# Kernel tuning notes

Hardware: AMD Instinct MI355X
Metric: run time of the kernel (lower is better)

## Reference

```python
import jax, jax.numpy as jnp
import numpy as np

B, NC, D, H, W = 2, 5, 96, 160, 160


def setup_inputs() -> dict:
    key = jax.random.key(0)
    k1, k2, k3 = jax.random.split(key, 3)
    source_logits = jax.random.normal(k1, (B, NC, D, H, W), dtype=jnp.float32)
    target_logits = jax.random.normal(k2, (B, NC, D, H, W), dtype=jnp.float32)
    gt = jax.random.randint(k3, (B, 1, D, H, W), 0, NC, dtype=jnp.int64)
    return {"source_logits": source_logits, "target_logits": target_logits, "gt": gt}


def reference(source_logits, target_logits, gt):
    temperature = 2.0
    eps = 1e-6
    n_class = source_logits.shape[1]
    batch = source_logits.shape[0]

    g = gt[:, 0]  # [B, D, H, W]
    # one-hot over classes: [K, B, D, H, W] (K = n_class segment ids)
    onehot = (g[None] == jnp.arange(n_class)[:, None, None, None, None]).astype(source_logits.dtype)
    # total voxel count per class over the whole batch (matches torch.sum(gt == i))
    nvox = jnp.sum(onehot, axis=(1, 2, 3, 4))  # [K]

    # per-class, per-batch, per-channel masked sums: single pass instead of n_class passes
    s_sum = jnp.einsum('kbdhw,bcdhw->kbc', onehot, source_logits)  # [K, B, C]
    t_sum = jnp.einsum('kbdhw,bcdhw->kbc', onehot, target_logits)

    denom = (nvox + eps)[:, None, None]
    s_avg = s_sum[:, :, 1:] / denom  # [K, B, C-1] (channel 0 dropped as in original)
    t_avg = t_sum[:, :, 1:] / denom

    s_lp = jax.nn.log_softmax(s_avg / temperature, axis=-1)
    t_lp = jax.nn.log_softmax(t_avg / temperature, axis=-1)

    # KLDivLoss(reduction='batchmean', log_target=True): sum(exp(t)*(t-s)) / batch
    kl_st = jnp.sum(jnp.exp(t_lp) * (t_lp - s_lp), axis=(1, 2)) / batch  # per class
    kl_ts = jnp.sum(jnp.exp(s_lp) * (s_lp - t_lp), axis=(1, 2)) / batch

    return jnp.mean((kl_st + kl_ts) / 2.0)
```

## Files before the change

kernel.cpp:

```cpp
#include <hip/hip_runtime.h>

#define NCLASS 5
#define NB 2
#define VOX (96*160*160)
#define V4  (VOX/4)
#define SLOTS 64
#define VALS  110
#define STAGP 1271


__global__ __launch_bounds__(256)
void kd_partial(const float* __restrict__ src, const float* __restrict__ tgt,
                const int* __restrict__ gt, float* __restrict__ ws)
{
    const int nbPerB = gridDim.x >> 1;
    const int b      = blockIdx.x / nbPerB;
    const int blk    = blockIdx.x - b * nbPerB;

    const float* sb = src + (size_t)b * NCLASS * VOX;
    const float* tb = tgt + (size_t)b * NCLASS * VOX;
    const int*   gb = gt  + (size_t)b * VOX;

    float accS[NCLASS][NCLASS];
    float accT[NCLASS][NCLASS];
    float cnt[NCLASS];
    #pragma unroll
    for (int k = 0; k < NCLASS; ++k) {
        cnt[k] = 0.f;
        #pragma unroll
        for (int c = 0; c < NCLASS; ++c) { accS[k][c] = 0.f; accT[k][c] = 0.f; }
    }

    const int tid    = blk * 256 + threadIdx.x;
    const int stride = nbPerB * 256;

    for (int i = tid; i < V4; i += stride) {
        #pragma unroll
        for (int c = 0; c < NCLASS; ++c) {
            int ic = i + c * STAGP;
            if (ic >= V4) ic -= V4;
            const int4   g4 = ((const int4*)gb)[ic];
            const float4 s4 = ((const float4*)(sb + (size_t)c * VOX))[ic];
            const float4 t4 = ((const float4*)(tb + (size_t)c * VOX))[ic];

            #define ACC_COMP(GX, SX, TX)                                     \
                { _Pragma("unroll")                                          \
                  for (int kk = 0; kk < NCLASS; ++kk) {                      \
                      const float m = ((GX) == kk) ? 1.0f : 0.0f;            \
                      accS[kk][c] = fmaf(m, (SX), accS[kk][c]);              \
                      accT[kk][c] = fmaf(m, (TX), accT[kk][c]);              \
                  } }
            ACC_COMP(g4.x, s4.x, t4.x)
            ACC_COMP(g4.y, s4.y, t4.y)
            ACC_COMP(g4.z, s4.z, t4.z)
            ACC_COMP(g4.w, s4.w, t4.w)
            #undef ACC_COMP

            if (c == 0) {
                #pragma unroll
                for (int kk = 0; kk < NCLASS; ++kk) {
                    cnt[kk] += ((g4.x == kk) ? 1.f : 0.f) + ((g4.y == kk) ? 1.f : 0.f)
                             + ((g4.z == kk) ? 1.f : 0.f) + ((g4.w == kk) ? 1.f : 0.f);
                }
            }
        }
    }

    __shared__ float lacc[55];
    const int lane = threadIdx.x & 63;
    if (threadIdx.x < 55) lacc[threadIdx.x] = 0.f;
    __syncthreads();

    #define WAVE_RED(VAL, IDX) {                                             \
        float v_ = (VAL);                                                    \
        _Pragma("unroll")                                                    \
        for (int off_ = 32; off_; off_ >>= 1) v_ += __shfl_xor(v_, off_);    \
        if (lane == 0) atomicAdd(&lacc[(IDX)], v_);                          \
    }
    #pragma unroll
    for (int k = 0; k < NCLASS; ++k) {
        #pragma unroll
        for (int c = 0; c < NCLASS; ++c) {
            WAVE_RED(accS[k][c], k * 5 + c);
            WAVE_RED(accT[k][c], 25 + k * 5 + c);
        }
        WAVE_RED(cnt[k], 50 + k);
    }
    #undef WAVE_RED
    __syncthreads();

    if (threadIdx.x < 55) {
        const int i = threadIdx.x;
        int gidx;
        if (i < 25)       gidx = b * 25 + i;
        else if (i < 50)  gidx = 50 + b * 25 + (i - 25);
        else              gidx = 100 + b * 5 + (i - 50);
        atomicAdd(&ws[(blockIdx.x & (SLOTS - 1)) * VALS + gidx], lacc[i]);
    }
}

__global__ void kd_final(const float* __restrict__ ws, float* __restrict__ out)
{
    const int tid = threadIdx.x;
    __shared__ float tot[VALS];

    for (int v = tid; v < VALS; v += 64) {
        float s = 0.f;
        #pragma unroll 8
        for (int slot = 0; slot < SLOTS; ++slot) s += ws[slot * VALS + v];
        tot[v] = s;
    }
    __syncthreads();

    const int l = (tid < 40) ? tid : 0;
    const int g = l >> 2;
    const int k = g >> 1;
    const int b = g & 1;
    const int c = l & 3;

    const double denom = (double)tot[100 + 0 * 5 + k]
                       + (double)tot[100 + 1 * 5 + k] + 1e-6;
    double sa = ((double)tot[(b * 5 + k) * 5 + (c + 1)] / denom) * 0.5;
    double ta = ((double)tot[50 + (b * 5 + k) * 5 + (c + 1)] / denom) * 0.5;

    double ms = sa, mt = ta;
    ms = fmax(ms, __shfl_xor(ms, 1)); ms = fmax(ms, __shfl_xor(ms, 2));
    mt = fmax(mt, __shfl_xor(mt, 1)); mt = fmax(mt, __shfl_xor(mt, 2));
    double es = exp(sa - ms), et = exp(ta - mt);
    es += __shfl_xor(es, 1); es += __shfl_xor(es, 2);
    et += __shfl_xor(et, 1); et += __shfl_xor(et, 2);
    const double slp = sa - (ms + log(es));
    const double tlp = ta - (mt + log(et));

    double term = exp(tlp) * (tlp - slp) + exp(slp) * (slp - tlp);
    if (tid >= 40) term = 0.0;

    #pragma unroll
    for (int off = 32; off; off >>= 1) term += __shfl_xor(term, off);
    if (tid == 0) out[0] = (float)(term / 20.0);
}

extern "C" void kernel_launch(void* const* d_in, const int* in_sizes, int n_in,
                              void* d_out, int out_size, void* d_ws, size_t ws_size,
                              hipStream_t stream)
{
    const float* src = (const float*)d_in[0];
    const float* tgt = (const float*)d_in[1];
    const int*   gt  = (const int*)d_in[2];
    float* out = (float*)d_out;
    float* ws  = (float*)d_ws;

    hipMemsetAsync(ws, 0, SLOTS * VALS * sizeof(float), stream);
    kd_partial<<<dim3(2048), dim3(256), 0, stream>>>(src, tgt, gt, ws);
    kd_final<<<dim3(1), dim3(64), 0, stream>>>(ws, out);
}
```

Baseline: 280.1 us.

## Split work per (batch, channel) slab to cut per-thread accumulators

```diff
diff --git a/kernel.cpp b/kernel.cpp
--- a/kernel.cpp
+++ b/kernel.cpp
@@ -6,96 +6,84 @@
 #define V4  (VOX/4)
 #define SLOTS 64
 #define VALS  110
-#define STAGP 1271
+#define BLKS_PER_SLAB 256
 
 
 __global__ __launch_bounds__(256)
 void kd_partial(const float* __restrict__ src, const float* __restrict__ tgt,
                 const int* __restrict__ gt, float* __restrict__ ws)
 {
-    const int nbPerB = gridDim.x >> 1;
-    const int b      = blockIdx.x / nbPerB;
-    const int blk    = blockIdx.x - b * nbPerB;
+    const int b = blockIdx.y / NCLASS;
+    const int c = blockIdx.y % NCLASS;
 
-    const float* sb = src + (size_t)b * NCLASS * VOX;
-    const float* tb = tgt + (size_t)b * NCLASS * VOX;
+    const float* sb = src + ((size_t)b * NCLASS + c) * VOX;
+    const float* tb = tgt + ((size_t)b * NCLASS + c) * VOX;
     const int*   gb = gt  + (size_t)b * VOX;
 
-    float accS[NCLASS][NCLASS];
-    float accT[NCLASS][NCLASS];
-    float cnt[NCLASS];
-    #pragma unroll
-    for (int k = 0; k < NCLASS; ++k) {
-        cnt[k] = 0.f;
-        #pragma unroll
-        for (int c = 0; c < NCLASS; ++c) { accS[k][c] = 0.f; accT[k][c] = 0.f; }
-    }
+    float accS[NCLASS] = {0.f, 0.f, 0.f, 0.f, 0.f};
+    float accT[NCLASS] = {0.f, 0.f, 0.f, 0.f, 0.f};
+    float cnt[NCLASS]  = {0.f, 0.f, 0.f, 0.f, 0.f};
 
-    const int tid    = blk * 256 + threadIdx.x;
-    const int stride = nbPerB * 256;
+    const int tid    = blockIdx.x * 256 + threadIdx.x;
+    const int stride = BLKS_PER_SLAB * 256;
 
-    for (int i = tid; i < V4; i += stride) {
-        #pragma unroll
-        for (int c = 0; c < NCLASS; ++c) {
-            int ic = i + c * STAGP;
-            if (ic >= V4) ic -= V4;
-            const int4   g4 = ((const int4*)gb)[ic];
-            const float4 s4 = ((const float4*)(sb + (size_t)c * VOX))[ic];
-            const float4 t4 = ((const float4*)(tb + (size_t)c * VOX))[ic];
+    #define BODY(WITH_CNT)                                                    \
+        for (int i = tid; i < V4; i += stride) {                              \
+            const int4   g4 = ((const int4*)gb)[i];                           \
+            const float4 s4 = ((const float4*)sb)[i];                         \
+            const float4 t4 = ((const float4*)tb)[i];                         \
+            _Pragma("unroll")                                                 \
+            for (int kk = 0; kk < NCLASS; ++kk) {                             \
+                const float mx = (g4.x == kk) ? 1.f : 0.f;                    \
+                const float my = (g4.y == kk) ? 1.f : 0.f;                    \
+                const float mz = (g4.z == kk) ? 1.f : 0.f;                    \
+                const float mw = (g4.w == kk) ? 1.f : 0.f;                    \
+                accS[kk] = fmaf(mx, s4.x, accS[kk]);                          \
+                accS[kk] = fmaf(my, s4.y, accS[kk]);                          \
+                accS[kk] = fmaf(mz, s4.z, accS[kk]);                          \
+                accS[kk] = fmaf(mw, s4.w, accS[kk]);                          \
+                accT[kk] = fmaf(mx, t4.x, accT[kk]);                          \
+                accT[kk] = fmaf(my, t4.y, accT[kk]);                          \
+                accT[kk] = fmaf(mz, t4.z, accT[kk]);                          \
+                accT[kk] = fmaf(mw, t4.w, accT[kk]);                          \
+                if (WITH_CNT) cnt[kk] += mx + my + mz + mw;                   \
+            }                                                                 \
+        }
+    if (c == 0) { BODY(1) } else { BODY(0) }
+    #undef BODY
 
-            #define ACC_COMP(GX, SX, TX)                                     \
-                { _Pragma("unroll")                                          \
-                  for (int kk = 0; kk < NCLASS; ++kk) {                      \
-                      const float m = ((GX) == kk) ? 1.0f : 0.0f;            \
-                      accS[kk][c] = fmaf(m, (SX), accS[kk][c]);              \
-                      accT[kk][c] = fmaf(m, (TX), accT[kk][c]);              \
-                  } }
-            ACC_COMP(g4.x, s4.x, t4.x)
-            ACC_COMP(g4.y, s4.y, t4.y)
-            ACC_COMP(g4.z, s4.z, t4.z)
-            ACC_COMP(g4.w, s4.w, t4.w)
-            #undef ACC_COMP
-
-            if (c == 0) {
-                #pragma unroll
-                for (int kk = 0; kk < NCLASS; ++kk) {
-                    cnt[kk] += ((g4.x == kk) ? 1.f : 0.f) + ((g4.y == kk) ? 1.f : 0.f)
-                             + ((g4.z == kk) ? 1.f : 0.f) + ((g4.w == kk) ? 1.f : 0.f);
-                }
-            }
-        }
-    }
-
-    __shared__ float lacc[55];
+    __shared__ float lacc[15];
     const int lane = threadIdx.x & 63;
-    if (threadIdx.x < 55) lacc[threadIdx.x] = 0.f;
+    if (threadIdx.x < 15) lacc[threadIdx.x] = 0.f;
     __syncthreads();
 
-    #define WAVE_RED(VAL, IDX) {                                             \
-        float v_ = (VAL);                                                    \
-        _Pragma("unroll")                                                    \
-        for (int off_ = 32; off_; off_ >>= 1) v_ += __shfl_xor(v_, off_);    \
-        if (lane == 0) atomicAdd(&lacc[(IDX)], v_);                          \
+    #define WAVE_RED(VAL, IDX) {                                              \
+        float v_ = (VAL);                                                     \
+        _Pragma("unroll")                                                     \
+        for (int off_ = 32; off_; off_ >>= 1) v_ += __shfl_xor(v_, off_);     \
+        if (lane == 0) atomicAdd(&lacc[(IDX)], v_);                           \
     }
     #pragma unroll
-    for (int k = 0; k < NCLASS; ++k) {
+    for (int kk = 0; kk < NCLASS; ++kk) {
+        WAVE_RED(accS[kk], kk);
+        WAVE_RED(accT[kk], 5 + kk);
+    }
+    if (c == 0) {
         #pragma unroll
-        for (int c = 0; c < NCLASS; ++c) {
-            WAVE_RED(accS[k][c], k * 5 + c);
-            WAVE_RED(accT[k][c], 25 + k * 5 + c);
-        }
-        WAVE_RED(cnt[k], 50 + k);
+        for (int kk = 0; kk < NCLASS; ++kk) WAVE_RED(cnt[kk], 10 + kk);
     }
     #undef WAVE_RED
     __syncthreads();
 
-    if (threadIdx.x < 55) {
-        const int i = threadIdx.x;
-        int gidx;
-        if (i < 25)       gidx = b * 25 + i;
-        else if (i < 50)  gidx = 50 + b * 25 + (i - 25);
-        else              gidx = 100 + b * 5 + (i - 50);
-        atomicAdd(&ws[(blockIdx.x & (SLOTS - 1)) * VALS + gidx], lacc[i]);
+    const int slot = (blockIdx.x + blockIdx.y * 37) & (SLOTS - 1);
+    if (threadIdx.x < 15) {
+        const int i  = threadIdx.x;
+        const int kk = i % 5;
+        int gidx = -1;
+        if (i < 5)        gidx = (b * 5 + kk) * 5 + c;
+        else if (i < 10)  gidx = 50 + (b * 5 + kk) * 5 + c;
+        else if (c == 0)  gidx = 100 + b * 5 + kk;
+        if (gidx >= 0) atomicAdd(&ws[slot * VALS + gidx], lacc[i]);
     }
 }
 
@@ -151,6 +139,6 @@
     float* ws  = (float*)d_ws;
 
     hipMemsetAsync(ws, 0, SLOTS * VALS * sizeof(float), stream);
-    kd_partial<<<dim3(2048), dim3(256), 0, stream>>>(src, tgt, gt, ws);
+    kd_partial<<<dim3(BLKS_PER_SLAB, NB * NCLASS), dim3(256), 0, stream>>>(src, tgt, gt, ws);
     kd_final<<<dim3(1), dim3(64), 0, stream>>>(ws, out);
 }
```

Result: faster. 237.6 us (-15.2%).
